# Kernel optimization log

Hardware: AMD Instinct MI355X
Metric: run time of the kernel (lower is better)

The kernel has to match this reference:

```python
import jax, jax.numpy as jnp
import numpy as np

B, D, H = 8, 512, 8
HD = D // H            # 64 head dim
NS, NT = 8192, 4096    # search / template points
ATTN_EPS = 1e-6
LN_EPS = 1e-5


def layer_norm(x, g, b):
    m = jnp.mean(x, axis=-1, keepdims=True)
    v = jnp.mean((x - m) ** 2, axis=-1, keepdims=True)
    return (x - m) * jax.lax.rsqrt(v + LN_EPS) * g + b


def setup_inputs() -> dict:
    key = jax.random.key(0)
    ks = jax.random.split(key, 20)
    s = 0.02
    return {
        "search_feat": jax.random.normal(ks[0], (B, D, NS), jnp.float32),
        "search_xyz": jax.random.uniform(ks[1], (B, NS, 3), jnp.float32),
        "template_feat": jax.random.normal(ks[2], (B, D, NT), jnp.float32),
        "template_xyz": jax.random.uniform(ks[3], (B, NT, 3), jnp.float32),
        "pos_w1": jax.random.normal(ks[4], (3, D), jnp.float32) * s,
        "pos_b1": jnp.zeros((D,), jnp.float32),
        "pos_w2": jax.random.normal(ks[5], (D, D), jnp.float32) * s,
        "pos_b2": jnp.zeros((D,), jnp.float32),
        "wq": jax.random.normal(ks[6], (D, D), jnp.float32) * s,
        "wk": jax.random.normal(ks[7], (D, D), jnp.float32) * s,
        "wv": jax.random.normal(ks[8], (D, D), jnp.float32) * s,
        "w_merge": jax.random.normal(ks[9], (D, D), jnp.float32) * s,
        "mlp_w1": jax.random.normal(ks[10], (2 * D, 2 * D), jnp.float32) * s,
        "mlp_w2": jax.random.normal(ks[11], (2 * D, D), jnp.float32) * s,
        "ln1_g": jnp.ones((D,), jnp.float32),
        "ln1_b": jnp.zeros((D,), jnp.float32),
        "ln2_g": jnp.ones((D,), jnp.float32),
        "ln2_b": jnp.zeros((D,), jnp.float32),
    }


def reference(search_feat, search_xyz, template_feat, template_xyz,
              pos_w1, pos_b1, pos_w2, pos_b2, wq, wk, wv, w_merge,
              mlp_w1, mlp_w2, ln1_g, ln1_b, ln2_g, ln2_b):
    bs = search_feat.shape[0]
    sf = jnp.transpose(search_feat, (0, 2, 1))    # [B, Ns, D]
    tf = jnp.transpose(template_feat, (0, 2, 1))  # [B, Nt, D]

    # positional MLP on template coordinates
    pos = jax.nn.relu(template_xyz @ pos_w1 + pos_b1) @ pos_w2 + pos_b2
    tf_pos = tf + pos

    q = (sf @ wq).reshape(bs, NS, H, HD)
    k = (tf @ wk).reshape(bs, NT, H, HD)
    v = (tf_pos @ wv).reshape(bs, NT, H, HD)

    # LoFTR-style linear attention: phi(x) = elu(x) + 1
    Q = jax.nn.elu(q) + 1.0
    K = jax.nn.elu(k) + 1.0
    v_len = v.shape[1]
    v_n = v / v_len
    KV = jnp.einsum("bshd,bshv->bhdv", K, v_n)                 # [B,H,d,d]
    Z = 1.0 / (jnp.einsum("blhd,bhd->blh", Q, K.sum(axis=1)) + ATTN_EPS)
    msg = jnp.einsum("blhd,bhdv->blhv", Q, KV) * Z[..., None] * v_len

    msg = msg.reshape(bs, NS, H * HD) @ w_merge
    msg = layer_norm(msg, ln1_g, ln1_b)
    cat = jnp.concatenate([sf, msg], axis=2)                    # [B,Ns,2D]
    msg = jax.nn.relu(cat @ mlp_w1) @ mlp_w2
    msg = layer_norm(msg, ln2_g, ln2_b)
    return jnp.transpose(sf + msg, (0, 2, 1))                   # [B,D,Ns]
```

## Files before the change

### kernel.cpp

```cpp
#include <hip/hip_runtime.h>
#include <stdint.h>
#include <stddef.h>


using ushort_t = unsigned short;
using short8 = __attribute__((ext_vector_type(8))) short;
using f32x4  = __attribute__((ext_vector_type(4))) float;

#define DEVI __device__ __forceinline__

DEVI float b2f(unsigned short u) {
    unsigned v = ((unsigned)u) << 16;
    return __builtin_bit_cast(float, v);
}
DEVI unsigned short f2b(float x) {
    unsigned u = __builtin_bit_cast(unsigned, x);
    u += 0x7FFFu + ((u >> 16) & 1u);
    return (unsigned short)(u >> 16);
}
DEVI void gload16(const void* g, void* l) {
    __builtin_amdgcn_global_load_lds(
        (const __attribute__((address_space(1))) unsigned*)g,
        (__attribute__((address_space(3))) unsigned*)l, 16, 0, 0);
}

template <int EPI>
__global__ __launch_bounds__(256, 3)
void gemm_bf16(const ushort_t* __restrict__ A0, const ushort_t* __restrict__ A1,
               const ushort_t* __restrict__ Wt, ushort_t* __restrict__ C,
               const float* __restrict__ bias, const ushort_t* __restrict__ addm,
               int N, int K, int K0, int lda0, int lda1, int nn)
{
    __shared__ ushort_t As[2][128 * 32];
    __shared__ ushort_t Bs[2][128 * 32];
    const int tid = threadIdx.x;
    const int cpx = gridDim.x >> 3;
    const int lid = (blockIdx.x & 7) * cpx + (blockIdx.x >> 3);
    const int m0 = (lid / nn) * 128;
    const int n0 = (lid % nn) * 128;
    const int w = tid >> 6, l = tid & 63;
    const int wm = (w >> 1) * 64, wn = (w & 1) * 64;
    const int lr = l & 15, lg = l >> 4;
    const int srow = tid >> 2;
    const int scol = ((tid & 3) ^ ((tid >> 3) & 3)) * 8;
    const int ka = (lg ^ ((lr >> 1) & 3)) * 8;

    f32x4 acc[4][4] = {};
    const int nk = K / 32;

    auto stage = [&](int kt, int buf) {
        const int kb = kt * 32;
        const ushort_t* asrc; int ld;
        if (kb < K0) { asrc = A0 + (size_t)m0 * lda0 + kb; ld = lda0; }
        else         { asrc = A1 + (size_t)m0 * lda1 + (kb - K0); ld = lda1; }
#pragma unroll
        for (int i = 0; i < 2; i++)
            gload16(asrc + (size_t)(i * 64 + srow) * ld + scol,
                    (void*)(&As[buf][i * 2048] + tid * 8));
        const ushort_t* wsrc = Wt + (size_t)n0 * K + kb;
#pragma unroll
        for (int i = 0; i < 2; i++)
            gload16(wsrc + (size_t)(i * 64 + srow) * K + scol,
                    (void*)(&Bs[buf][i * 2048] + tid * 8));
    };

    stage(0, 0);
    __syncthreads();
    for (int kt = 0; kt < nk; ++kt) {
        const int cur = kt & 1;
        if (kt + 1 < nk) stage(kt + 1, cur ^ 1);
        short8 a[4], b[4];
#pragma unroll
        for (int mf = 0; mf < 4; mf++)
            a[mf] = *(const short8*)&As[cur][(wm + mf * 16 + lr) * 32 + ka];
#pragma unroll
        for (int nf = 0; nf < 4; nf++)
            b[nf] = *(const short8*)&Bs[cur][(wn + nf * 16 + lr) * 32 + ka];
#pragma unroll
        for (int mf = 0; mf < 4; mf++)
#pragma unroll
            for (int nf = 0; nf < 4; nf++)
                acc[mf][nf] = __builtin_amdgcn_mfma_f32_16x16x32_bf16(
                    a[mf], b[nf], acc[mf][nf], 0, 0, 0);
        __syncthreads();
    }

#pragma unroll
    for (int mf = 0; mf < 4; mf++) {
#pragma unroll
        for (int i = 0; i < 4; i++) {
            const int m = m0 + wm + mf * 16 + lg * 4 + i;
#pragma unroll
            for (int nf = 0; nf < 4; nf++) {
                const int n = n0 + wn + nf * 16 + lr;
                float x = acc[mf][nf][i];
                if constexpr (EPI == 1) { x = x > 0.f ? x + 1.f : __expf(x); }
                if constexpr (EPI == 2) { x += bias[n] + b2f(addm[(size_t)m * N + n]); }
                if constexpr (EPI == 3) { x = fmaxf(x, 0.f); }
                C[(size_t)m * N + n] = f2b(x);
            }
        }
    }
}

__global__ __launch_bounds__(256)
void transpose_f32_bf16(const float* __restrict__ in, ushort_t* __restrict__ out,
                        int R, int Cc)
{
    __shared__ float tile[64][65];
    const int t = threadIdx.x;
    const int c0 = blockIdx.x * 64, r0 = blockIdx.y * 64;
    const size_t bo = (size_t)blockIdx.z * (size_t)R * (size_t)Cc;
    const float* src = in + bo;
    ushort_t* dst = out + bo;
#pragma unroll
    for (int i = 0; i < 4; i++) {
        const int r = (t >> 4) + i * 16;
        const int c = (t & 15) * 4;
        const float4 v = *(const float4*)&src[(size_t)(r0 + r) * Cc + c0 + c];
        tile[r][c + 0] = v.x; tile[r][c + 1] = v.y;
        tile[r][c + 2] = v.z; tile[r][c + 3] = v.w;
    }
    __syncthreads();
#pragma unroll
    for (int i = 0; i < 2; i++) {
        const int c = (t >> 3) + i * 32;
        const int rs = (t & 7) * 8;
        short8 o;
#pragma unroll
        for (int j = 0; j < 8; j++) o[j] = (short)f2b(tile[rs + j][c]);
        *(short8*)&dst[(size_t)(c0 + c) * R + r0 + rs] = o;
    }
}

__global__ __launch_bounds__(256)
void pos_mlp1(const float* __restrict__ xyz, const float* __restrict__ w1,
              const float* __restrict__ b1, ushort_t* __restrict__ P1)
{
    const int t = threadIdx.x;
    const int m = blockIdx.x * 4 + (t >> 6);
    const int n0 = (t & 63) * 8;
    const float x = xyz[m * 3 + 0], y = xyz[m * 3 + 1], z = xyz[m * 3 + 2];
    short8 o;
#pragma unroll
    for (int j = 0; j < 8; j++) {
        const int n = n0 + j;
        float v = x * w1[n] + y * w1[512 + n] + z * w1[1024 + n] + b1[n];
        o[j] = (short)f2b(fmaxf(v, 0.f));
    }
    *(short8*)&P1[(size_t)m * 512 + n0] = o;
}

__global__ __launch_bounds__(256)
void kv_partial(const ushort_t* __restrict__ Kp, const ushort_t* __restrict__ V,
                float* __restrict__ KVp, float* __restrict__ Ksp)
{
    __shared__ ushort_t Ks[256 * 64];
    __shared__ ushort_t Vs[256 * 64];
    const int t = threadIdx.x;
    const int sp = blockIdx.x, h = blockIdx.y, b = blockIdx.z;
    const int d0 = t >> 2, e0 = (t & 3) * 16;
    const int srow = t >> 3, scol = (t & 7) * 8;
    float acc[16] = {};
    float ksum = 0.f;
    for (int c = 0; c < 4; c++) {
        if (c) __syncthreads();
        const size_t sbase = (size_t)b * 4096 + sp * 1024 + c * 256;
#pragma unroll
        for (int i = 0; i < 8; i++) {
            const size_t go = (sbase + i * 32 + srow) * 512 + h * 64 + scol;
            gload16(Kp + go, (void*)(&Ks[i * 2048] + t * 8));
            gload16(V + go, (void*)(&Vs[i * 2048] + t * 8));
        }
        __syncthreads();
        for (int s = 0; s < 256; s++) {
            const float k = b2f(Ks[s * 64 + d0]);
            if ((t & 3) == 0) ksum += k;
            const short8 v0 = *(const short8*)&Vs[s * 64 + e0];
            const short8 v1 = *(const short8*)&Vs[s * 64 + e0 + 8];
#pragma unroll
            for (int j = 0; j < 8; j++) {
                acc[j]     += k * b2f((unsigned short)v0[j]);
                acc[8 + j] += k * b2f((unsigned short)v1[j]);
            }
        }
    }
    const int bh = b * 8 + h;
    float* kvo = KVp + (((size_t)sp * 64 + bh) * 64 + d0) * 64 + e0;
#pragma unroll
    for (int j = 0; j < 16; j++) kvo[j] = acc[j];
    if ((t & 3) == 0) Ksp[((size_t)sp * 64 + bh) * 64 + d0] = ksum;
}

__global__ __launch_bounds__(256)
void kv_finalize(const float* __restrict__ KVp, const float* __restrict__ Ksp,
                 ushort_t* __restrict__ KVt, float* __restrict__ Ksum)
{
    const int bh = blockIdx.x, t = threadIdx.x;
#pragma unroll
    for (int i = 0; i < 16; i++) {
        const int idx = i * 256 + t;
        const int e = idx >> 6, d = idx & 63;
        float s = 0.f;
#pragma unroll
        for (int sp = 0; sp < 4; sp++)
            s += KVp[(((size_t)sp * 64 + bh) * 64 + d) * 64 + e];
        KVt[(size_t)bh * 4096 + idx] = f2b(s);
    }
    if (t < 64) {
        float s = 0.f;
#pragma unroll
        for (int sp = 0; sp < 4; sp++) s += Ksp[((size_t)sp * 64 + bh) * 64 + t];
        Ksum[(size_t)bh * 64 + t] = s;
    }
}

__global__ __launch_bounds__(256)
void z_comp(const ushort_t* __restrict__ Qp, const float* __restrict__ Ksum,
            float* __restrict__ Z)
{
    const int t = threadIdx.x;
    const int row = blockIdx.x * 32 + (t >> 3);
    const int h = t & 7;
    const int b = row >> 13;
    const ushort_t* q = Qp + (size_t)row * 512 + h * 64;
    const float* ks = Ksum + ((size_t)b * 8 + h) * 64;
    float s = 0.f;
#pragma unroll
    for (int j0 = 0; j0 < 64; j0 += 8) {
        const short8 v = *(const short8*)&q[j0];
#pragma unroll
        for (int j = 0; j < 8; j++) s += b2f((unsigned short)v[j]) * ks[j0 + j];
    }
    Z[(size_t)row * 8 + h] = 1.f / (s + 1e-6f);
}

__global__ __launch_bounds__(256, 2)
void attn_apply(const ushort_t* __restrict__ Qp, const ushort_t* __restrict__ KVt,
                const float* __restrict__ Z, ushort_t* __restrict__ msg1)
{
    __shared__ ushort_t As[256 * 64];
    __shared__ ushort_t Bs[64 * 64];
    const int t = threadIdx.x;
    const int ch = blockIdx.x, h = blockIdx.y, b = blockIdx.z;
    const int w = t >> 6, l = t & 63;
    const int lr = l & 15, lg = l >> 4;
    const int row0 = ch * 256;
    const int srow = t >> 3;
    const int scol = ((t & 7) ^ ((t >> 3) & 7)) * 8;
    const ushort_t* kv = KVt + (size_t)(b * 8 + h) * 4096;
#pragma unroll
    for (int i = 0; i < 2; i++)
        gload16(kv + (size_t)(i * 32 + srow) * 64 + scol,
                (void*)(&Bs[i * 2048] + t * 8));
    const ushort_t* qb = Qp + ((size_t)b * 8192 + row0) * 512 + h * 64;
#pragma unroll
    for (int i = 0; i < 8; i++)
        gload16(qb + (size_t)(i * 32 + srow) * 512 + scol,
                (void*)(&As[i * 2048] + t * 8));
    __syncthreads();
    f32x4 acc[4][4] = {};
    const int wr = w * 64;
#pragma unroll
    for (int ks = 0; ks < 2; ks++) {
        const int cb = ks * 4 + lg;
        const int kswz = (cb ^ (lr & 7)) * 8;
        short8 a[4], bb[4];
#pragma unroll
        for (int mf = 0; mf < 4; mf++)
            a[mf] = *(const short8*)&As[(wr + mf * 16 + lr) * 64 + kswz];
#pragma unroll
        for (int nf = 0; nf < 4; nf++)
            bb[nf] = *(const short8*)&Bs[(nf * 16 + lr) * 64 + kswz];
#pragma unroll
        for (int mf = 0; mf < 4; mf++)
#pragma unroll
            for (int nf = 0; nf < 4; nf++)
                acc[mf][nf] = __builtin_amdgcn_mfma_f32_16x16x32_bf16(
                    a[mf], bb[nf], acc[mf][nf], 0, 0, 0);
    }
#pragma unroll
    for (int mf = 0; mf < 4; mf++) {
#pragma unroll
        for (int i = 0; i < 4; i++) {
            const int m = row0 + wr + mf * 16 + lg * 4 + i;
            const float z = Z[((size_t)b * 8192 + m) * 8 + h];
#pragma unroll
            for (int nf = 0; nf < 4; nf++) {
                const int e = nf * 16 + lr;
                msg1[((size_t)b * 8192 + m) * 512 + h * 64 + e] =
                    f2b(acc[mf][nf][i] * z);
            }
        }
    }
}

__global__ __launch_bounds__(256)
void layer_norm_k(ushort_t* __restrict__ X, const float* __restrict__ g,
                  const float* __restrict__ bta)
{
    const int t = threadIdx.x;
    const int row = blockIdx.x * 4 + (t >> 6);
    const int l = t & 63;
    ushort_t* x = X + (size_t)row * 512;
    const short8 v = *(const short8*)&x[l * 8];
    float f[8];
    float s = 0.f;
#pragma unroll
    for (int j = 0; j < 8; j++) { f[j] = b2f((unsigned short)v[j]); s += f[j]; }
#pragma unroll
    for (int o = 32; o > 0; o >>= 1) s += __shfl_xor(s, o);
    const float mean = s * (1.f / 512.f);
    float vs = 0.f;
#pragma unroll
    for (int j = 0; j < 8; j++) { const float d = f[j] - mean; vs += d * d; }
#pragma unroll
    for (int o = 32; o > 0; o >>= 1) vs += __shfl_xor(vs, o);
    const float rstd = rsqrtf(vs * (1.f / 512.f) + 1e-5f);
    short8 ov;
#pragma unroll
    for (int j = 0; j < 8; j++) {
        const int c = l * 8 + j;
        ov[j] = (short)f2b((f[j] - mean) * rstd * g[c] + bta[c]);
    }
    *(short8*)&x[l * 8] = ov;
}

__global__ __launch_bounds__(256)
void final_out(const float* __restrict__ sfeat, const ushort_t* __restrict__ msgf,
               float* __restrict__ out)
{
    __shared__ float tile[64][65];
    const int t = threadIdx.x;
    const int ns0 = blockIdx.x * 64, d0 = blockIdx.y * 64, b = blockIdx.z;
#pragma unroll
    for (int ii = 0; ii < 2; ii++) {
        const int nsl = (t >> 3) + ii * 32, ds = (t & 7) * 8;
        const short8 v =
            *(const short8*)&msgf[((size_t)b * 8192 + ns0 + nsl) * 512 + d0 + ds];
#pragma unroll
        for (int j = 0; j < 8; j++) tile[ds + j][nsl] = b2f((unsigned short)v[j]);
    }
    __syncthreads();
#pragma unroll
    for (int i = 0; i < 4; i++) {
        const int d = (t >> 4) + i * 16;
        const int nss = (t & 15) * 4;
        const size_t off = ((size_t)b * 512 + d0 + d) * 8192 + ns0 + nss;
        const float4 sv = *(const float4*)&sfeat[off];
        float4 o;
        o.x = sv.x + tile[d][nss + 0];
        o.y = sv.y + tile[d][nss + 1];
        o.z = sv.z + tile[d][nss + 2];
        o.w = sv.w + tile[d][nss + 3];
        *(float4*)&out[off] = o;
    }
}

extern "C" void kernel_launch(void* const* d_in, const int* in_sizes, int n_in,
                              void* d_out, int out_size, void* d_ws, size_t ws_size,
                              hipStream_t stream)
{
    (void)in_sizes; (void)n_in; (void)out_size; (void)ws_size;
    const float* search_feat   = (const float*)d_in[0];
    const float* template_feat = (const float*)d_in[2];
    const float* template_xyz  = (const float*)d_in[3];
    const float* pos_w1  = (const float*)d_in[4];
    const float* pos_b1  = (const float*)d_in[5];
    const float* pos_w2  = (const float*)d_in[6];
    const float* pos_b2  = (const float*)d_in[7];
    const float* wq      = (const float*)d_in[8];
    const float* wk      = (const float*)d_in[9];
    const float* wv      = (const float*)d_in[10];
    const float* w_merge = (const float*)d_in[11];
    const float* mlp_w1  = (const float*)d_in[12];
    const float* mlp_w2  = (const float*)d_in[13];
    const float* ln1_g   = (const float*)d_in[14];
    const float* ln1_b   = (const float*)d_in[15];
    const float* ln2_g   = (const float*)d_in[16];
    const float* ln2_b   = (const float*)d_in[17];
    float* out = (float*)d_out;

    char* ws = (char*)d_ws;
    ushort_t* sfT    = (ushort_t*)(ws + 0);
    ushort_t* Qp     = (ushort_t*)(ws + 67108864);
    ushort_t* tfT    = (ushort_t*)(ws + 134217728);
    ushort_t* Kp     = (ushort_t*)(ws + 167772160);
    ushort_t* msg2   = (ushort_t*)(ws + 134217728);
    ushort_t* P1     = (ushort_t*)(ws + 201326592);
    ushort_t* Vv     = (ushort_t*)(ws + 201326592);
    ushort_t* tfpos  = (ushort_t*)(ws + 234881024);
    ushort_t* msg1   = (ushort_t*)(ws + 268435456);
    ushort_t* hidden = (ushort_t*)(ws + 201326592);
    ushort_t* outp   = Qp;
    ushort_t* wqT  = (ushort_t*)(ws + 335544320);
    ushort_t* wkT  = (ushort_t*)(ws + 336068608);
    ushort_t* wvT  = (ushort_t*)(ws + 336592896);
    ushort_t* wmT  = (ushort_t*)(ws + 337117184);
    ushort_t* pw2T = (ushort_t*)(ws + 337641472);
    ushort_t* w1T  = (ushort_t*)(ws + 338165760);
    ushort_t* w2T  = (ushort_t*)(ws + 340262912);
    float*    KVp  = (float*)(ws + 341311488);
    float*    Ksp  = (float*)(ws + 345505792);
    ushort_t* KVt  = (ushort_t*)(ws + 345571328);
    float*    Ksum = (float*)(ws + 346095616);
    float*    Zbuf = (float*)(ws + 346112000);

    transpose_f32_bf16<<<dim3(128, 8, 8), 256, 0, stream>>>(search_feat, sfT, 512, 8192);
    transpose_f32_bf16<<<dim3(64, 8, 8), 256, 0, stream>>>(template_feat, tfT, 512, 4096);
    transpose_f32_bf16<<<dim3(8, 8, 1), 256, 0, stream>>>(wq, wqT, 512, 512);
    transpose_f32_bf16<<<dim3(8, 8, 1), 256, 0, stream>>>(wk, wkT, 512, 512);
    transpose_f32_bf16<<<dim3(8, 8, 1), 256, 0, stream>>>(wv, wvT, 512, 512);
    transpose_f32_bf16<<<dim3(8, 8, 1), 256, 0, stream>>>(w_merge, wmT, 512, 512);
    transpose_f32_bf16<<<dim3(8, 8, 1), 256, 0, stream>>>(pos_w2, pw2T, 512, 512);
    transpose_f32_bf16<<<dim3(16, 16, 1), 256, 0, stream>>>(mlp_w1, w1T, 1024, 1024);
    transpose_f32_bf16<<<dim3(8, 16, 1), 256, 0, stream>>>(mlp_w2, w2T, 1024, 512);

    gemm_bf16<1><<<dim3(2048), 256, 0, stream>>>(sfT, nullptr, wqT, Qp,
                                                 nullptr, nullptr, 512, 512, 512, 512, 0, 4);
    gemm_bf16<1><<<dim3(1024), 256, 0, stream>>>(tfT, nullptr, wkT, Kp,
                                                 nullptr, nullptr, 512, 512, 512, 512, 0, 4);
    pos_mlp1<<<dim3(8192), 256, 0, stream>>>(template_xyz, pos_w1, pos_b1, P1);
    gemm_bf16<2><<<dim3(1024), 256, 0, stream>>>(P1, nullptr, pw2T, tfpos,
                                                 pos_b2, tfT, 512, 512, 512, 512, 0, 4);
    gemm_bf16<0><<<dim3(1024), 256, 0, stream>>>(tfpos, nullptr, wvT, Vv,
                                                 nullptr, nullptr, 512, 512, 512, 512, 0, 4);
    kv_partial<<<dim3(4, 8, 8), 256, 0, stream>>>(Kp, Vv, KVp, Ksp);
    kv_finalize<<<dim3(64), 256, 0, stream>>>(KVp, Ksp, KVt, Ksum);
    z_comp<<<dim3(2048), 256, 0, stream>>>(Qp, Ksum, Zbuf);
    attn_apply<<<dim3(32, 8, 8), 256, 0, stream>>>(Qp, KVt, Zbuf, msg1);
    gemm_bf16<0><<<dim3(2048), 256, 0, stream>>>(msg1, nullptr, wmT, msg2,
                                                 nullptr, nullptr, 512, 512, 512, 512, 0, 4);
    layer_norm_k<<<dim3(16384), 256, 0, stream>>>(msg2, ln1_g, ln1_b);
    gemm_bf16<3><<<dim3(4096), 256, 0, stream>>>(sfT, msg2, w1T, hidden,
                                                 nullptr, nullptr, 1024, 1024, 512, 512, 512, 8);
    gemm_bf16<0><<<dim3(2048), 256, 0, stream>>>(hidden, nullptr, w2T, outp,
                                                 nullptr, nullptr, 512, 1024, 1024, 1024, 0, 4);
    layer_norm_k<<<dim3(16384), 256, 0, stream>>>(outp, ln2_g, ln2_b);
    final_out<<<dim3(128, 8, 8), 256, 0, stream>>>(search_feat, outp, out);
}
```

Measured before the change: 772.0 us.

## Retile GEMM to 128x256 triple-buffered pipeline, fold Z into attention, fuse LN2 with output

The GEMM now uses 512-thread blocks with 128x256 tiles, a K-step of 64 and a three-stage LDS ring buffer. Loads are split across the two half-steps, with explicit vmcnt waits and raised MFMA priority to overlap global traffic with compute. The key-sum vector is appended as an extra row to the KV matrix so attn_apply computes the normaliser as a fifth MFMA column, which removes the z_comp kernel and its Z buffer. The second layer norm, residual add and transpose are fused into one kernel that reads the bf16 search features instead of the fp32 input. The exchange is more LDS per block, fewer resident blocks, and bf16 rounding of the residual and the key sum.

```diff
diff --git a/kernel.cpp b/kernel.cpp
--- a/kernel.cpp
+++ b/kernel.cpp
@@ -25,64 +25,96 @@
 }
 
 template <int EPI>
-__global__ __launch_bounds__(256, 3)
+__global__ __launch_bounds__(512, 1)
 void gemm_bf16(const ushort_t* __restrict__ A0, const ushort_t* __restrict__ A1,
                const ushort_t* __restrict__ Wt, ushort_t* __restrict__ C,
                const float* __restrict__ bias, const ushort_t* __restrict__ addm,
                int N, int K, int K0, int lda0, int lda1, int nn)
 {
-    __shared__ ushort_t As[2][128 * 32];
-    __shared__ ushort_t Bs[2][128 * 32];
+    __shared__ ushort_t As[3][128 * 64];
+    __shared__ ushort_t Bs[3][256 * 64];
     const int tid = threadIdx.x;
     const int cpx = gridDim.x >> 3;
     const int lid = (blockIdx.x & 7) * cpx + (blockIdx.x >> 3);
     const int m0 = (lid / nn) * 128;
-    const int n0 = (lid % nn) * 128;
+    const int n0 = (lid % nn) * 256;
     const int w = tid >> 6, l = tid & 63;
-    const int wm = (w >> 1) * 64, wn = (w & 1) * 64;
+    const int wm = (w >> 2) * 64;
+    const int wn = (w & 3) * 64;
     const int lr = l & 15, lg = l >> 4;
-    const int srow = tid >> 2;
-    const int scol = ((tid & 3) ^ ((tid >> 3) & 3)) * 8;
-    const int ka = (lg ^ ((lr >> 1) & 3)) * 8;
+    const int str = tid >> 3;
+    const int sc  = ((tid & 7) ^ (str & 7)) * 8;
+    const int nk = K / 64;
 
     f32x4 acc[4][4] = {};
-    const int nk = K / 32;
-
-    auto stage = [&](int kt, int buf) {
-        const int kb = kt * 32;
+
+    auto stageA = [&](int kt, int buf) {
+        const int kb = kt * 64;
         const ushort_t* asrc; int ld;
         if (kb < K0) { asrc = A0 + (size_t)m0 * lda0 + kb; ld = lda0; }
         else         { asrc = A1 + (size_t)m0 * lda1 + (kb - K0); ld = lda1; }
 #pragma unroll
-        for (int i = 0; i < 2; i++)
-            gload16(asrc + (size_t)(i * 64 + srow) * ld + scol,
-                    (void*)(&As[buf][i * 2048] + tid * 8));
+        for (int j = 0; j < 2; j++)
+            gload16(asrc + (size_t)(j * 64 + str) * ld + sc,
+                    (void*)(&As[buf][j * 4096] + tid * 8));
+    };
+    auto stageB = [&](int kt, int buf) {
+        const int kb = kt * 64;
         const ushort_t* wsrc = Wt + (size_t)n0 * K + kb;
 #pragma unroll
-        for (int i = 0; i < 2; i++)
-            gload16(wsrc + (size_t)(i * 64 + srow) * K + scol,
-                    (void*)(&Bs[buf][i * 2048] + tid * 8));
+        for (int j = 0; j < 4; j++)
+            gload16(wsrc + (size_t)(j * 64 + str) * K + sc,
+                    (void*)(&Bs[buf][j * 4096] + tid * 8));
     };
 
-    stage(0, 0);
-    __syncthreads();
-    for (int kt = 0; kt < nk; ++kt) {
-        const int cur = kt & 1;
-        if (kt + 1 < nk) stage(kt + 1, cur ^ 1);
-        short8 a[4], b[4];
-#pragma unroll
-        for (int mf = 0; mf < 4; mf++)
-            a[mf] = *(const short8*)&As[cur][(wm + mf * 16 + lr) * 32 + ka];
-#pragma unroll
-        for (int nf = 0; nf < 4; nf++)
-            b[nf] = *(const short8*)&Bs[cur][(wn + nf * 16 + lr) * 32 + ka];
-#pragma unroll
-        for (int mf = 0; mf < 4; mf++)
+    stageA(0, 0); stageB(0, 0);
+    stageA(1, 1); stageB(1, 1);
+    asm volatile("s_waitcnt vmcnt(6)" ::: "memory");
+    __builtin_amdgcn_s_barrier();
+
+    for (int t = 0; t < nk; ++t) {
+        const int cur = t % 3;
+        const int nxt = (t + 2) % 3;
+        const bool pre = (t + 2) < nk;
+        {
+            short8 a[4], b[4];
+#pragma unroll
+            for (int mf = 0; mf < 4; mf++)
+                a[mf] = *(const short8*)&As[cur][(wm + mf * 16 + lr) * 64 + ((lg) ^ (lr & 7)) * 8];
 #pragma unroll
             for (int nf = 0; nf < 4; nf++)
-                acc[mf][nf] = __builtin_amdgcn_mfma_f32_16x16x32_bf16(
-                    a[mf], b[nf], acc[mf][nf], 0, 0, 0);
-        __syncthreads();
+                b[nf] = *(const short8*)&Bs[cur][(wn + nf * 16 + lr) * 64 + ((lg) ^ (lr & 7)) * 8];
+            if (pre) stageA(t + 2, nxt);
+            __builtin_amdgcn_s_setprio(1);
+#pragma unroll
+            for (int mf = 0; mf < 4; mf++)
+#pragma unroll
+                for (int nf = 0; nf < 4; nf++)
+                    acc[mf][nf] = __builtin_amdgcn_mfma_f32_16x16x32_bf16(
+                        a[mf], b[nf], acc[mf][nf], 0, 0, 0);
+            __builtin_amdgcn_s_setprio(0);
+        }
+        {
+            short8 a[4], b[4];
+#pragma unroll
+            for (int mf = 0; mf < 4; mf++)
+                a[mf] = *(const short8*)&As[cur][(wm + mf * 16 + lr) * 64 + ((4 + lg) ^ (lr & 7)) * 8];
+#pragma unroll
+            for (int nf = 0; nf < 4; nf++)
+                b[nf] = *(const short8*)&Bs[cur][(wn + nf * 16 + lr) * 64 + ((4 + lg) ^ (lr & 7)) * 8];
+            if (pre) stageB(t + 2, nxt);
+            __builtin_amdgcn_s_setprio(1);
+#pragma unroll
+            for (int mf = 0; mf < 4; mf++)
+#pragma unroll
+                for (int nf = 0; nf < 4; nf++)
+                    acc[mf][nf] = __builtin_amdgcn_mfma_f32_16x16x32_bf16(
+                        a[mf], b[nf], acc[mf][nf], 0, 0, 0);
+            __builtin_amdgcn_s_setprio(0);
+        }
+        if (pre) { asm volatile("s_waitcnt vmcnt(6)" ::: "memory"); }
+        else     { asm volatile("s_waitcnt vmcnt(0)" ::: "memory"); }
+        __builtin_amdgcn_s_barrier();
     }
 
 #pragma unroll
@@ -194,9 +226,10 @@
 
 __global__ __launch_bounds__(256)
 void kv_finalize(const float* __restrict__ KVp, const float* __restrict__ Ksp,
-                 ushort_t* __restrict__ KVt, float* __restrict__ Ksum)
+                 ushort_t* __restrict__ KVt)
 {
     const int bh = blockIdx.x, t = threadIdx.x;
+    ushort_t* o = KVt + (size_t)bh * 5120;
 #pragma unroll
     for (int i = 0; i < 16; i++) {
         const int idx = i * 256 + t;
@@ -205,77 +238,60 @@
 #pragma unroll
         for (int sp = 0; sp < 4; sp++)
             s += KVp[(((size_t)sp * 64 + bh) * 64 + d) * 64 + e];
-        KVt[(size_t)bh * 4096 + idx] = f2b(s);
+        o[idx] = f2b(s);
     }
     if (t < 64) {
         float s = 0.f;
 #pragma unroll
         for (int sp = 0; sp < 4; sp++) s += Ksp[((size_t)sp * 64 + bh) * 64 + t];
-        Ksum[(size_t)bh * 64 + t] = s;
-    }
-}
-
-__global__ __launch_bounds__(256)
-void z_comp(const ushort_t* __restrict__ Qp, const float* __restrict__ Ksum,
-            float* __restrict__ Z)
-{
-    const int t = threadIdx.x;
-    const int row = blockIdx.x * 32 + (t >> 3);
-    const int h = t & 7;
-    const int b = row >> 13;
-    const ushort_t* q = Qp + (size_t)row * 512 + h * 64;
-    const float* ks = Ksum + ((size_t)b * 8 + h) * 64;
-    float s = 0.f;
-#pragma unroll
-    for (int j0 = 0; j0 < 64; j0 += 8) {
-        const short8 v = *(const short8*)&q[j0];
-#pragma unroll
-        for (int j = 0; j < 8; j++) s += b2f((unsigned short)v[j]) * ks[j0 + j];
-    }
-    Z[(size_t)row * 8 + h] = 1.f / (s + 1e-6f);
+        o[4096 + t] = f2b(s);
+    }
+    for (int idx = 4160 + t; idx < 5120; idx += 256) o[idx] = 0;
 }
 
 __global__ __launch_bounds__(256, 2)
 void attn_apply(const ushort_t* __restrict__ Qp, const ushort_t* __restrict__ KVt,
-                const float* __restrict__ Z, ushort_t* __restrict__ msg1)
+                ushort_t* __restrict__ msg1)
 {
     __shared__ ushort_t As[256 * 64];
-    __shared__ ushort_t Bs[64 * 64];
+    __shared__ ushort_t Bs[80 * 64];
     const int t = threadIdx.x;
     const int ch = blockIdx.x, h = blockIdx.y, b = blockIdx.z;
     const int w = t >> 6, l = t & 63;
     const int lr = l & 15, lg = l >> 4;
     const int row0 = ch * 256;
     const int srow = t >> 3;
-    const int scol = ((t & 7) ^ ((t >> 3) & 7)) * 8;
-    const ushort_t* kv = KVt + (size_t)(b * 8 + h) * 4096;
+    const int sc = ((t & 7) ^ (srow & 7)) * 8;
+    const ushort_t* kv = KVt + (size_t)(b * 8 + h) * 5120;
 #pragma unroll
     for (int i = 0; i < 2; i++)
-        gload16(kv + (size_t)(i * 32 + srow) * 64 + scol,
+        gload16(kv + (size_t)(i * 32 + srow) * 64 + sc,
                 (void*)(&Bs[i * 2048] + t * 8));
+    if (t < 128)
+        gload16(kv + (size_t)(64 + srow) * 64 + sc,
+                (void*)(&Bs[4096] + t * 8));
     const ushort_t* qb = Qp + ((size_t)b * 8192 + row0) * 512 + h * 64;
 #pragma unroll
     for (int i = 0; i < 8; i++)
-        gload16(qb + (size_t)(i * 32 + srow) * 512 + scol,
+        gload16(qb + (size_t)(i * 32 + srow) * 512 + sc,
                 (void*)(&As[i * 2048] + t * 8));
     __syncthreads();
-    f32x4 acc[4][4] = {};
+    f32x4 acc[4][5] = {};
     const int wr = w * 64;
 #pragma unroll
     for (int ks = 0; ks < 2; ks++) {
-        const int cb = ks * 4 + lg;
-        const int kswz = (cb ^ (lr & 7)) * 8;
-        short8 a[4], bb[4];
+        const int kswz = ((ks * 4 + lg) ^ (lr & 7)) * 8;
+        short8 a[4], bb[5];
 #pragma unroll
         for (int mf = 0; mf < 4; mf++)
             a[mf] = *(const short8*)&As[(wr + mf * 16 + lr) * 64 + kswz];
 #pragma unroll
-        for (int nf = 0; nf < 4; nf++)
+        for (int nf = 0; nf < 5; nf++)
             bb[nf] = *(const short8*)&Bs[(nf * 16 + lr) * 64 + kswz];
 #pragma unroll
         for (int mf = 0; mf < 4; mf++)
 #pragma unroll
-            for (int nf = 0; nf < 4; nf++)
+            for (int nf = 0; nf < 5; nf++)
                 acc[mf][nf] = __builtin_amdgcn_mfma_f32_16x16x32_bf16(
                     a[mf], bb[nf], acc[mf][nf], 0, 0, 0);
     }
@@ -284,7 +300,8 @@
 #pragma unroll
         for (int i = 0; i < 4; i++) {
             const int m = row0 + wr + mf * 16 + lg * 4 + i;
-            const float z = Z[((size_t)b * 8192 + m) * 8 + h];
+            const float zden = __shfl(acc[mf][4][i], (l & 48));
+            const float z = 1.f / (zden + 1e-6f);
 #pragma unroll
             for (int nf = 0; nf < 4; nf++) {
                 const int e = nf * 16 + lr;
@@ -327,33 +344,53 @@
 }
 
 __global__ __launch_bounds__(256)
-void final_out(const float* __restrict__ sfeat, const ushort_t* __restrict__ msgf,
+void ln2_final(const ushort_t* __restrict__ outp, const ushort_t* __restrict__ sfT,
+               const float* __restrict__ g, const float* __restrict__ bta,
                float* __restrict__ out)
 {
-    __shared__ float tile[64][65];
-    const int t = threadIdx.x;
-    const int ns0 = blockIdx.x * 64, d0 = blockIdx.y * 64, b = blockIdx.z;
-#pragma unroll
-    for (int ii = 0; ii < 2; ii++) {
-        const int nsl = (t >> 3) + ii * 32, ds = (t & 7) * 8;
-        const short8 v =
-            *(const short8*)&msgf[((size_t)b * 8192 + ns0 + nsl) * 512 + d0 + ds];
-#pragma unroll
-        for (int j = 0; j < 8; j++) tile[ds + j][nsl] = b2f((unsigned short)v[j]);
+    __shared__ ushort_t tile[64][514];
+    const int t = threadIdx.x;
+    const int ns0 = blockIdx.x * 64, b = blockIdx.y;
+    const int w = t >> 6, l = t & 63;
+#pragma unroll
+    for (int rr = 0; rr < 16; rr++) {
+        const int r = w * 16 + rr;
+        const size_t grow = (size_t)b * 8192 + ns0 + r;
+        const short8 v = *(const short8*)&outp[grow * 512 + l * 8];
+        float f[8];
+        float s = 0.f;
+#pragma unroll
+        for (int j = 0; j < 8; j++) { f[j] = b2f((unsigned short)v[j]); s += f[j]; }
+#pragma unroll
+        for (int o = 32; o > 0; o >>= 1) s += __shfl_xor(s, o);
+        const float mean = s * (1.f / 512.f);
+        float vs = 0.f;
+#pragma unroll
+        for (int j = 0; j < 8; j++) { const float d = f[j] - mean; vs += d * d; }
+#pragma unroll
+        for (int o = 32; o > 0; o >>= 1) vs += __shfl_xor(vs, o);
+        const float rstd = rsqrtf(vs * (1.f / 512.f) + 1e-5f);
+        const short8 sv = *(const short8*)&sfT[grow * 512 + l * 8];
+        short8 ov;
+#pragma unroll
+        for (int j = 0; j < 8; j++) {
+            const int c = l * 8 + j;
+            ov[j] = (short)f2b(b2f((unsigned short)sv[j]) +
+                               (f[j] - mean) * rstd * g[c] + bta[c]);
+        }
+        *(short8*)&tile[r][l * 8] = ov;
     }
     __syncthreads();
 #pragma unroll
-    for (int i = 0; i < 4; i++) {
+    for (int i = 0; i < 32; i++) {
         const int d = (t >> 4) + i * 16;
         const int nss = (t & 15) * 4;
-        const size_t off = ((size_t)b * 512 + d0 + d) * 8192 + ns0 + nss;
-        const float4 sv = *(const float4*)&sfeat[off];
         float4 o;
-        o.x = sv.x + tile[d][nss + 0];
-        o.y = sv.y + tile[d][nss + 1];
-        o.z = sv.z + tile[d][nss + 2];
-        o.w = sv.w + tile[d][nss + 3];
-        *(float4*)&out[off] = o;
+        o.x = b2f(tile[nss + 0][d]);
+        o.y = b2f(tile[nss + 1][d]);
+        o.z = b2f(tile[nss + 2][d]);
+        o.w = b2f(tile[nss + 3][d]);
+        *(float4*)&out[((size_t)b * 512 + d) * 8192 + ns0 + nss] = o;
     }
 }
 
@@ -403,8 +440,6 @@
     float*    KVp  = (float*)(ws + 341311488);
     float*    Ksp  = (float*)(ws + 345505792);
     ushort_t* KVt  = (ushort_t*)(ws + 345571328);
-    float*    Ksum = (float*)(ws + 346095616);
-    float*    Zbuf = (float*)(ws + 346112000);
 
     transpose_f32_bf16<<<dim3(128, 8, 8), 256, 0, stream>>>(search_feat, sfT, 512, 8192);
     transpose_f32_bf16<<<dim3(64, 8, 8), 256, 0, stream>>>(template_feat, tfT, 512, 4096);
@@ -416,26 +451,24 @@
     transpose_f32_bf16<<<dim3(16, 16, 1), 256, 0, stream>>>(mlp_w1, w1T, 1024, 1024);
     transpose_f32_bf16<<<dim3(8, 16, 1), 256, 0, stream>>>(mlp_w2, w2T, 1024, 512);
 
-    gemm_bf16<1><<<dim3(2048), 256, 0, stream>>>(sfT, nullptr, wqT, Qp,
-                                                 nullptr, nullptr, 512, 512, 512, 512, 0, 4);
-    gemm_bf16<1><<<dim3(1024), 256, 0, stream>>>(tfT, nullptr, wkT, Kp,
-                                                 nullptr, nullptr, 512, 512, 512, 512, 0, 4);
+    gemm_bf16<1><<<dim3(1024), 512, 0, stream>>>(sfT, nullptr, wqT, Qp,
+                                                 nullptr, nullptr, 512, 512, 512, 512, 0, 2);
+    gemm_bf16<1><<<dim3(512), 512, 0, stream>>>(tfT, nullptr, wkT, Kp,
+                                                nullptr, nullptr, 512, 512, 512, 512, 0, 2);
     pos_mlp1<<<dim3(8192), 256, 0, stream>>>(template_xyz, pos_w1, pos_b1, P1);
-    gemm_bf16<2><<<dim3(1024), 256, 0, stream>>>(P1, nullptr, pw2T, tfpos,
-                                                 pos_b2, tfT, 512, 512, 512, 512, 0, 4);
-    gemm_bf16<0><<<dim3(1024), 256, 0, stream>>>(tfpos, nullptr, wvT, Vv,
-                                                 nullptr, nullptr, 512, 512, 512, 512, 0, 4);
+    gemm_bf16<2><<<dim3(512), 512, 0, stream>>>(P1, nullptr, pw2T, tfpos,
+                                                pos_b2, tfT, 512, 512, 512, 512, 0, 2);
+    gemm_bf16<0><<<dim3(512), 512, 0, stream>>>(tfpos, nullptr, wvT, Vv,
+                                                nullptr, nullptr, 512, 512, 512, 512, 0, 2);
     kv_partial<<<dim3(4, 8, 8), 256, 0, stream>>>(Kp, Vv, KVp, Ksp);
-    kv_finalize<<<dim3(64), 256, 0, stream>>>(KVp, Ksp, KVt, Ksum);
-    z_comp<<<dim3(2048), 256, 0, stream>>>(Qp, Ksum, Zbuf);
-    attn_apply<<<dim3(32, 8, 8), 256, 0, stream>>>(Qp, KVt, Zbuf, msg1);
-    gemm_bf16<0><<<dim3(2048), 256, 0, stream>>>(msg1, nullptr, wmT, msg2,
-                                                 nullptr, nullptr, 512, 512, 512, 512, 0, 4);
+    kv_finalize<<<dim3(64), 256, 0, stream>>>(KVp, Ksp, KVt);
+    attn_apply<<<dim3(32, 8, 8), 256, 0, stream>>>(Qp, KVt, msg1);
+    gemm_bf16<0><<<dim3(1024), 512, 0, stream>>>(msg1, nullptr, wmT, msg2,
+                                                 nullptr, nullptr, 512, 512, 512, 512, 0, 2);
     layer_norm_k<<<dim3(16384), 256, 0, stream>>>(msg2, ln1_g, ln1_b);
-    gemm_bf16<3><<<dim3(4096), 256, 0, stream>>>(sfT, msg2, w1T, hidden,
-                                                 nullptr, nullptr, 1024, 1024, 512, 512, 512, 8);
-    gemm_bf16<0><<<dim3(2048), 256, 0, stream>>>(hidden, nullptr, w2T, outp,
-                                                 nullptr, nullptr, 512, 1024, 1024, 1024, 0, 4);
-    layer_norm_k<<<dim3(16384), 256, 0, stream>>>(outp, ln2_g, ln2_b);
-    final_out<<<dim3(128, 8, 8), 256, 0, stream>>>(search_feat, outp, out);
-}
+    gemm_bf16<3><<<dim3(2048), 512, 0, stream>>>(sfT, msg2, w1T, hidden,
+                                                 nullptr, nullptr, 1024, 1024, 512, 512, 512, 4);
+    gemm_bf16<0><<<dim3(1024), 512, 0, stream>>>(hidden, nullptr, w2T, outp,
+                                                 nullptr, nullptr, 512, 1024, 1024, 1024, 0, 2);
+    ln2_final<<<dim3(128, 8), 256, 0, stream>>>(outp, sfT, ln2_g, ln2_b, out);
+}
```

After: 760.1 us. No clear change (-1.5%).
